# Performance work log

Measured on AMD Instinct MI355X. Metric: run time of the kernel, lower is better.

Reference implementation:

```python
import jax, jax.numpy as jnp
import numpy as np

N_MODES = 64


def setup_inputs() -> dict:
    key = jax.random.key(0)
    ks = jax.random.split(key, 5)
    B, L, C, M = 32, 8192, 64, N_MODES
    scale = 1.0 / (C * M)
    return {
        "x": jax.random.normal(ks[0], (B, L, C), dtype=jnp.float32),
        "w_spec_real": jax.random.normal(ks[1], (C, C, M), dtype=jnp.float32) * scale,
        "w_spec_imag": jax.random.normal(ks[2], (C, C, M), dtype=jnp.float32) * scale,
        "pw_weight": jax.random.normal(ks[3], (C, C), dtype=jnp.float32) * (1.0 / np.sqrt(C)),
        "pw_bias": jax.random.normal(ks[4], (C,), dtype=jnp.float32) * 0.01,
    }


def reference(x, w_spec_real, w_spec_imag, pw_weight, pw_bias):
    # x: [B, L, C] -> [B, C, L] (matches torch transpose(1, 2))
    xt = jnp.swapaxes(x, 1, 2)
    L = xt.shape[-1]
    xf = jnp.fft.rfft(xt, axis=-1)            # [B, C, F] complex64, F = L//2 + 1
    F = xf.shape[-1]
    K = min(N_MODES, F)
    W = (w_spec_real + 1j * w_spec_imag).astype(xf.dtype)  # [Cin, Cout, M]
    # Batched replacement of the per-mode loop: [B,Cin,K] x [Cin,Cout,K] -> [B,Cout,K]
    tf_low = jnp.einsum('bik,iok->bok', xf[:, :, :K], W[:, :, :K])
    tf = jnp.zeros_like(xf).at[:, :, :K].set(tf_low)
    x_back = jnp.fft.irfft(tf, n=L, axis=-1)  # [B, C, L] real
    # pointwise conv (kernel_size=1): [Cout,Cin] x [B,Cin,L] + bias
    pw = jnp.einsum('oi,bil->bol', pw_weight, xt) + pw_bias[None, :, None]
    return jnp.swapaxes(x_back + pw, 1, 2)     # [B, L, C]
```

## Files before the change

### kernel.cpp

```cpp
#include <hip/hip_runtime.h>
#include <stdint.h>

#define L_     8192
#define NB     32
#define NC     64
#define SPLITK 16
#define CHUNK  (L_ / SPLITK)
#define SXPAD  520

#define BF_OFF  0
#define XF_OFF  (2u  << 20)
#define XR_OFF  (18u << 20)
#define WC_OFF  (19u << 20)

typedef __bf16 bf16x8 __attribute__((ext_vector_type(8)));
typedef float  f32x4  __attribute__((ext_vector_type(4)));

__device__ __forceinline__ unsigned short f2bf(float f) {
  union { float f; unsigned int i; } v; v.f = f;
  unsigned int r = v.i + 0x7fffu + ((v.i >> 16) & 1u);
  return (unsigned short)(r >> 16);
}
__device__ __forceinline__ f32x4 mfma16(bf16x8 a, bf16x8 b, f32x4 c) {
  return __builtin_amdgcn_mfma_f32_16x16x32_bf16(a, b, c, 0, 0, 0);
}

__global__ __launch_bounds__(256) void k0_bf(unsigned short* __restrict__ Bf,
                                             const uint2* __restrict__ wrsrc,
                                             uint2* __restrict__ wc) {
  const int t = blockIdx.x * 256 + threadIdx.x;
  const int e0 = t * 8;
  const int j = e0 >> 13, l0 = e0 & 8191, k = j >> 1;
  const float W0 = 6.283185307179586f / 8192.0f;
  const float a = (k == 0 ? 1.0f : 2.0f) * (1.0f / 8192.0f);
  uint32_t w[4];
  #pragma unroll
  for (int u = 0; u < 4; ++u) {
    float s0, c0, s1, c1;
    __sincosf((float)((k * (l0 + 2 * u)) & 8191) * W0, &s0, &c0);
    __sincosf((float)((k * (l0 + 2 * u + 1)) & 8191) * W0, &s1, &c1);
    const unsigned short b0 = f2bf((j & 1) ? (-a * s0) : (a * c0));
    const unsigned short b1 = f2bf((j & 1) ? (-a * s1) : (a * c1));
    w[u] = (uint32_t)b0 | ((uint32_t)b1 << 16);
  }
  uint4 v; v.x = w[0]; v.y = w[1]; v.z = w[2]; v.w = w[3];
  *(uint4*)(Bf + e0) = v;
  wc[t] = wrsrc[t];
}

__global__ __launch_bounds__(256) void k1_dft(const float* __restrict__ x,
                                              const unsigned short* __restrict__ Bf,
                                              float* __restrict__ XFP) {
  const int b = blockIdx.x >> 4;
  const int p = blockIdx.x & 15;
  const int l0 = p * CHUNK;
  const int t = threadIdx.x;
  const int wv = t >> 6, lane = t & 63, q = lane >> 4, n = lane & 15;
  __shared__ uint32_t sx[NC * SXPAD / 2];
  const float* xb = x + (size_t)b * L_ * NC;

  {
    const int g  = t & 15;
    const int r2 = t >> 4;
    for (int s = 0; s < 16; ++s) {
      const int lrow = s * 32 + 2 * r2;
      const f32x4 u0 = *(const f32x4*)(xb + (size_t)(l0 + lrow) * NC + 4 * g);
      const f32x4 u1 = *(const f32x4*)(xb + (size_t)(l0 + lrow + 1) * NC + 4 * g);
      #pragma unroll
      for (int jj = 0; jj < 4; ++jj) {
        __bf16 pk2[2] = {(__bf16)u0[jj], (__bf16)u1[jj]};
        sx[(4 * g + jj) * (SXPAD / 2) + s * 16 + r2] = __builtin_bit_cast(uint32_t, pk2);
      }
    }
  }
  __syncthreads();

  f32x4 acc[2][4];
  #pragma unroll
  for (int i = 0; i < 2; ++i)
    #pragma unroll
    for (int jn = 0; jn < 4; ++jn) acc[i][jn] = (f32x4){0.f, 0.f, 0.f, 0.f};
  const unsigned short* sxu = (const unsigned short*)sx;

  for (int ks = 0; ks < CHUNK; ks += 32) {
    const int lb = ks + q * 8;
    bf16x8 bfr[4];
    #pragma unroll
    for (int nt = 0; nt < 4; ++nt)
      bfr[nt] = *(const bf16x8*)(sxu + (nt * 16 + n) * SXPAD + lb);
    #pragma unroll
    for (int mt = 0; mt < 2; ++mt) {
      const bf16x8 afr = *(const bf16x8*)(Bf + (size_t)(wv * 32 + mt * 16 + n) * L_ + l0 + lb);
      #pragma unroll
      for (int nt = 0; nt < 4; ++nt)
        acc[mt][nt] = mfma16(afr, bfr[nt], acc[mt][nt]);
    }
  }

  float* op = XFP + (size_t)(p * NB + b) * 8192;
  #pragma unroll
  for (int mt = 0; mt < 2; ++mt)
    #pragma unroll
    for (int nt = 0; nt < 4; ++nt)
      *(f32x4*)(op + (size_t)(nt * 16 + n) * 128 + (wv * 32 + mt * 16 + q * 4)) =
          acc[mt][nt];
}

__global__ __launch_bounds__(256) void k1b_red(const f32x4* __restrict__ XFP,
                                               f32x4* __restrict__ XFR) {
  const int idx = blockIdx.x * 256 + threadIdx.x;
  f32x4 s = XFP[idx];
  #pragma unroll
  for (int p = 1; p < SPLITK; ++p) {
    const f32x4 v = XFP[(size_t)p * 65536 + idx];
    s[0] += v[0]; s[1] += v[1]; s[2] += v[2]; s[3] += v[3];
  }
  XFR[idx] = s;
}

__global__ __launch_bounds__(256) void k2_mix(const float* __restrict__ XFR,
                                              const float* __restrict__ wc,
                                              const float* __restrict__ wi,
                                              const float* __restrict__ pww,
                                              uint32_t* __restrict__ tf_out) {
  const int b = blockIdx.x >> 3;
  const int og = blockIdx.x & 7;
  const int t = threadIdx.x;
  const int k = t & 63;
  const int wv = t >> 6;
  __shared__ float sxf[8192];
  {
    f32x4* d = (f32x4*)sxf;
    const f32x4* s = (const f32x4*)(XFR + (size_t)b * 8192);
    #pragma unroll
    for (int i = 0; i < 8; ++i) d[t + i * 256] = s[t + i * 256];
  }
  __syncthreads();
  #pragma unroll
  for (int oo = 0; oo < 2; ++oo) {
    const int o = og * 8 + wv * 2 + oo;
    float ar = 0.f, ai = 0.f;
    #pragma unroll 8
    for (int i = 0; i < 64; ++i) {
      const float2 xv  = *(const float2*)&sxf[i * 128 + 2 * k];
      const float  wrv = wc[(size_t)i * 4096 + o * 64 + k];
      const float  wiv = wi[(size_t)i * 4096 + o * 64 + k];
      ar = fmaf(xv.x, wrv, ar);  ar = fmaf(-xv.y, wiv, ar);
      ai = fmaf(xv.x, wiv, ai);  ai = fmaf(xv.y, wrv, ai);
    }
    uint32_t* row = tf_out + ((size_t)b * 64 + o) * 96;
    row[k] = (uint32_t)f2bf(ar) | ((uint32_t)f2bf(ai) << 16);
    if (k < 32)
      row[64 + k] = (uint32_t)f2bf(pww[o * 64 + 2 * k]) |
                    ((uint32_t)f2bf(pww[o * 64 + 2 * k + 1]) << 16);
  }
}

__global__ __launch_bounds__(256) void k3_out(const float* __restrict__ x,
                                              const unsigned short* __restrict__ tf,
                                              const float* __restrict__ bias,
                                              float* __restrict__ out) {
  const int b = blockIdx.x >> 6;
  const int lt = blockIdx.x & 63;
  const int t = threadIdx.x;
  const int wv = t >> 6;
  const int lane = t & 63;
  const int q = lane >> 4;
  const int n = lane & 15;
  const int l0 = lt * 128 + wv * 32;
  const float* xb = x + (size_t)b * L_ * NC;
  const unsigned short* tfb = tf + (size_t)b * 64 * 192;
  const float W0 = 6.283185307179586f / 8192.0f;
  const int lA = l0 + n;
  const int lB = l0 + 16 + n;

  const f32x4* pA0 = (const f32x4*)(xb + (size_t)lA * NC + q * 8);
  const f32x4* pB0 = (const f32x4*)(xb + (size_t)lB * NC + q * 8);
  const f32x4* pA1 = (const f32x4*)(xb + (size_t)lA * NC + 32 + q * 8);
  const f32x4* pB1 = (const f32x4*)(xb + (size_t)lB * NC + 32 + q * 8);
  const f32x4 xA00 = pA0[0], xA01 = pA0[1];
  const f32x4 xB00 = pB0[0], xB01 = pB0[1];
  const f32x4 xA10 = pA1[0], xA11 = pA1[1];
  const f32x4 xB10 = pB1[0], xB11 = pB1[1];

  __shared__ unsigned short stf[64 * 200];
  {
    uint4* dst = (uint4*)stf;
    const uint4* src = (const uint4*)tfb;
    #pragma unroll
    for (int i = 0; i < 6; ++i) {
      const int e4 = t + i * 256;
      const int row = e4 / 24, c4 = e4 - row * 24;
      dst[row * 25 + c4] = src[e4];
    }
  }
  __syncthreads();

  f32x4 acc[4][2];
  #pragma unroll
  for (int i = 0; i < 4; ++i)
    #pragma unroll
    for (int jn = 0; jn < 2; ++jn) acc[i][jn] = (f32x4){0.f, 0.f, 0.f, 0.f};

  #pragma unroll
  for (int s = 0; s < 6; ++s) {
    const int k0 = s * 32;
    bf16x8 b0, b1;
    if (s < 4) {
      #pragma unroll
      for (int jj = 0; jj < 4; ++jj) {
        const int kf = (k0 >> 1) + q * 4 + jj;
        float sv, cv;
        __sincosf((float)((kf * lA) & 8191) * W0, &sv, &cv);
        b0[2 * jj] = (__bf16)cv; b0[2 * jj + 1] = (__bf16)(-sv);
        __sincosf((float)((kf * lB) & 8191) * W0, &sv, &cv);
        b1[2 * jj] = (__bf16)cv; b1[2 * jj + 1] = (__bf16)(-sv);
      }
    } else if (s == 4) {
      #pragma unroll
      for (int jj = 0; jj < 4; ++jj) {
        b0[jj] = (__bf16)xA00[jj]; b0[4 + jj] = (__bf16)xA01[jj];
        b1[jj] = (__bf16)xB00[jj]; b1[4 + jj] = (__bf16)xB01[jj];
      }
    } else {
      #pragma unroll
      for (int jj = 0; jj < 4; ++jj) {
        b0[jj] = (__bf16)xA10[jj]; b0[4 + jj] = (__bf16)xA11[jj];
        b1[jj] = (__bf16)xB10[jj]; b1[4 + jj] = (__bf16)xB11[jj];
      }
    }
    #pragma unroll
    for (int mt = 0; mt < 4; ++mt) {
      const bf16x8 afr = *(const bf16x8*)(stf + (mt * 16 + n) * 200 + k0 + q * 8);
      acc[mt][0] = mfma16(afr, b0, acc[mt][0]);
      acc[mt][1] = mfma16(afr, b1, acc[mt][1]);
    }
  }
  float* ob = out + (size_t)b * L_ * NC;
  #pragma unroll
  for (int mt = 0; mt < 4; ++mt) {
    const f32x4 bv = *(const f32x4*)(bias + mt * 16 + q * 4);
    #pragma unroll
    for (int nt = 0; nt < 2; ++nt) {
      const int l = l0 + nt * 16 + n;
      f32x4 v = acc[mt][nt];
      v[0] += bv[0]; v[1] += bv[1]; v[2] += bv[2]; v[3] += bv[3];
      *(f32x4*)(ob + (size_t)l * NC + mt * 16 + q * 4) = v;
    }
  }
}

extern "C" void kernel_launch(void* const* d_in, const int* in_sizes, int n_in,
                              void* d_out, int out_size, void* d_ws, size_t ws_size,
                              hipStream_t stream) {
  (void)in_sizes; (void)n_in; (void)out_size; (void)d_ws; (void)ws_size;
  const float* x    = (const float*)d_in[0];
  float*       wr   = (float*)d_in[1];
  const float* wi   = (const float*)d_in[2];
  const float* pww  = (const float*)d_in[3];
  const float* bias = (const float*)d_in[4];
  float* out = (float*)d_out;

  char* ob = (char*)d_out;
  unsigned short* Bf  = (unsigned short*)(ob + BF_OFF);
  float*          XFP = (float*)(ob + XF_OFF);
  float*          XFR = (float*)(ob + XR_OFF);
  float*          WC  = (float*)(ob + WC_OFF);

  k0_bf   <<<512,         256, 0, stream>>>(Bf, (const uint2*)wr, (uint2*)WC);
  k1_dft  <<<NB * SPLITK, 256, 0, stream>>>(x, Bf, XFP);
  k1b_red <<<256,         256, 0, stream>>>((const f32x4*)XFP, (f32x4*)XFR);
  k2_mix  <<<NB * 8,      256, 0, stream>>>(XFR, WC, wi, pww, (uint32_t*)wr);
  k3_out  <<<NB * 64,     256, 0, stream>>>(x, (const unsigned short*)wr, bias, out);
}
```

Measured before the change: 162.9 us.

## Generate DFT twiddles inline in MFMA loop and use workspace for spectral buffer

Removes the precomputed bf16 DFT basis table and its generator kernel; the DFT kernel now computes cosine twiddles on the fly (sine rows via a quarter-period phase offset) for each A fragment before the MFMAs. When a large enough workspace is provided, the mixed spectrum goes into the workspace instead of overwriting the weight input, which removes the weight copy kernel. This drops a launch and the global reads of the basis table, but adds transcendental ALU work inside the inner MFMA loop.

Measured after the change: 163.9 us. About the same (+0.6%).

```diff
diff --git a/kernel.cpp b/kernel.cpp
--- a/kernel.cpp
+++ b/kernel.cpp
@@ -8,10 +8,9 @@
 #define CHUNK  (L_ / SPLITK)
 #define SXPAD  520
 
-#define BF_OFF  0
-#define XF_OFF  (2u  << 20)
-#define XR_OFF  (18u << 20)
-#define WC_OFF  (19u << 20)
+#define XF_OFF  0
+#define XR_OFF  (16u << 20)
+#define WC_OFF  (17u << 20)
 
 typedef __bf16 bf16x8 __attribute__((ext_vector_type(8)));
 typedef float  f32x4  __attribute__((ext_vector_type(4)));
@@ -25,31 +24,7 @@
   return __builtin_amdgcn_mfma_f32_16x16x32_bf16(a, b, c, 0, 0, 0);
 }
 
-__global__ __launch_bounds__(256) void k0_bf(unsigned short* __restrict__ Bf,
-                                             const uint2* __restrict__ wrsrc,
-                                             uint2* __restrict__ wc) {
-  const int t = blockIdx.x * 256 + threadIdx.x;
-  const int e0 = t * 8;
-  const int j = e0 >> 13, l0 = e0 & 8191, k = j >> 1;
-  const float W0 = 6.283185307179586f / 8192.0f;
-  const float a = (k == 0 ? 1.0f : 2.0f) * (1.0f / 8192.0f);
-  uint32_t w[4];
-  #pragma unroll
-  for (int u = 0; u < 4; ++u) {
-    float s0, c0, s1, c1;
-    __sincosf((float)((k * (l0 + 2 * u)) & 8191) * W0, &s0, &c0);
-    __sincosf((float)((k * (l0 + 2 * u + 1)) & 8191) * W0, &s1, &c1);
-    const unsigned short b0 = f2bf((j & 1) ? (-a * s0) : (a * c0));
-    const unsigned short b1 = f2bf((j & 1) ? (-a * s1) : (a * c1));
-    w[u] = (uint32_t)b0 | ((uint32_t)b1 << 16);
-  }
-  uint4 v; v.x = w[0]; v.y = w[1]; v.z = w[2]; v.w = w[3];
-  *(uint4*)(Bf + e0) = v;
-  wc[t] = wrsrc[t];
-}
-
 __global__ __launch_bounds__(256) void k1_dft(const float* __restrict__ x,
-                                              const unsigned short* __restrict__ Bf,
                                               float* __restrict__ XFP) {
   const int b = blockIdx.x >> 4;
   const int p = blockIdx.x & 15;
@@ -82,19 +57,33 @@
     for (int jn = 0; jn < 4; ++jn) acc[i][jn] = (f32x4){0.f, 0.f, 0.f, 0.f};
   const unsigned short* sxu = (const unsigned short*)sx;
 
+  const float W0 = 6.283185307179586f / 8192.0f;
+  const int r0  = wv * 32 + n;
+  const int kr0 = r0 >> 1;
+  const int kr1 = kr0 + 8;
+  const int off = (r0 & 1) << 11;
+  const float a0s = (kr0 == 0 ? 1.0f : 2.0f) * (1.0f / 8192.0f);
+  const float a1s = 2.0f * (1.0f / 8192.0f);
+
   for (int ks = 0; ks < CHUNK; ks += 32) {
     const int lb = ks + q * 8;
     bf16x8 bfr[4];
     #pragma unroll
     for (int nt = 0; nt < 4; ++nt)
       bfr[nt] = *(const bf16x8*)(sxu + (nt * 16 + n) * SXPAD + lb);
-    #pragma unroll
-    for (int mt = 0; mt < 2; ++mt) {
-      const bf16x8 afr = *(const bf16x8*)(Bf + (size_t)(wv * 32 + mt * 16 + n) * L_ + l0 + lb);
-      #pragma unroll
-      for (int nt = 0; nt < 4; ++nt)
-        acc[mt][nt] = mfma16(afr, bfr[nt], acc[mt][nt]);
-    }
+    const int lbase = l0 + lb;
+    bf16x8 a0f, a1f;
+    #pragma unroll
+    for (int jj = 0; jj < 8; ++jj) {
+      a0f[jj] = (__bf16)(a0s * __cosf((float)((kr0 * (lbase + jj) + off) & 8191) * W0));
+      a1f[jj] = (__bf16)(a1s * __cosf((float)((kr1 * (lbase + jj) + off) & 8191) * W0));
+    }
+    #pragma unroll
+    for (int nt = 0; nt < 4; ++nt)
+      acc[0][nt] = mfma16(a0f, bfr[nt], acc[0][nt]);
+    #pragma unroll
+    for (int nt = 0; nt < 4; ++nt)
+      acc[1][nt] = mfma16(a1f, bfr[nt], acc[1][nt]);
   }
 
   float* op = XFP + (size_t)(p * NB + b) * 8192;
@@ -118,8 +107,15 @@
   XFR[idx] = s;
 }
 
+__global__ __launch_bounds__(256) void kwc_copy(const uint2* __restrict__ src,
+                                                uint2* __restrict__ dst) {
+  const int t = blockIdx.x * 256 + threadIdx.x;
+  dst[t] = src[t];
+  dst[t + 65536] = src[t + 65536];
+}
+
 __global__ __launch_bounds__(256) void k2_mix(const float* __restrict__ XFR,
-                                              const float* __restrict__ wc,
+                                              const float* __restrict__ wre,
                                               const float* __restrict__ wi,
                                               const float* __restrict__ pww,
                                               uint32_t* __restrict__ tf_out) {
@@ -143,7 +139,7 @@
     #pragma unroll 8
     for (int i = 0; i < 64; ++i) {
       const float2 xv  = *(const float2*)&sxf[i * 128 + 2 * k];
-      const float  wrv = wc[(size_t)i * 4096 + o * 64 + k];
+      const float  wrv = wre[(size_t)i * 4096 + o * 64 + k];
       const float  wiv = wi[(size_t)i * 4096 + o * 64 + k];
       ar = fmaf(xv.x, wrv, ar);  ar = fmaf(-xv.y, wiv, ar);
       ai = fmaf(xv.x, wiv, ai);  ai = fmaf(xv.y, wrv, ai);
@@ -253,7 +249,7 @@
 extern "C" void kernel_launch(void* const* d_in, const int* in_sizes, int n_in,
                               void* d_out, int out_size, void* d_ws, size_t ws_size,
                               hipStream_t stream) {
-  (void)in_sizes; (void)n_in; (void)out_size; (void)d_ws; (void)ws_size;
+  (void)in_sizes; (void)n_in; (void)out_size;
   const float* x    = (const float*)d_in[0];
   float*       wr   = (float*)d_in[1];
   const float* wi   = (const float*)d_in[2];
@@ -262,14 +258,17 @@
   float* out = (float*)d_out;
 
   char* ob = (char*)d_out;
-  unsigned short* Bf  = (unsigned short*)(ob + BF_OFF);
-  float*          XFP = (float*)(ob + XF_OFF);
-  float*          XFR = (float*)(ob + XR_OFF);
-  float*          WC  = (float*)(ob + WC_OFF);
-
-  k0_bf   <<<512,         256, 0, stream>>>(Bf, (const uint2*)wr, (uint2*)WC);
-  k1_dft  <<<NB * SPLITK, 256, 0, stream>>>(x, Bf, XFP);
+  float* XFP = (float*)(ob + XF_OFF);
+  float* XFR = (float*)(ob + XR_OFF);
+  float* WC  = (float*)(ob + WC_OFF);
+
+  const bool useWs = (d_ws != nullptr) && (ws_size >= (size_t)(768u * 1024u));
+  uint32_t* TFS = useWs ? (uint32_t*)d_ws : (uint32_t*)wr;
+  const float* wsrc = useWs ? wr : WC;
+
+  if (!useWs) kwc_copy<<<256, 256, 0, stream>>>((const uint2*)wr, (uint2*)WC);
+  k1_dft  <<<NB * SPLITK, 256, 0, stream>>>(x, XFP);
   k1b_red <<<256,         256, 0, stream>>>((const f32x4*)XFP, (f32x4*)XFR);
-  k2_mix  <<<NB * 8,      256, 0, stream>>>(XFR, WC, wi, pww, (uint32_t*)wr);
-  k3_out  <<<NB * 64,     256, 0, stream>>>(x, (const unsigned short*)wr, bias, out);
-}
+  k2_mix  <<<NB * 8,      256, 0, stream>>>(XFR, wsrc, wi, pww, TFS);
+  k3_out  <<<NB * 64,     256, 0, stream>>>(x, (const unsigned short*)TFS, bias, out);
+}
```
